# Performance work log

Hardware: AMD Instinct MI355X
Metric: run time of the kernel (lower is better)

The kernel has to match this reference:

```python
import jax, jax.numpy as jnp
import numpy as np

SLOPE = 25.0   # snntorch surrogate.fast_sigmoid default slope
THR = 1.0      # snntorch Leaky default threshold
BETA = 0.95
SPIKE_STEPS = 4
NUM_HEADS = 16

@jax.custom_vjp
def spike(u):
    # Heaviside forward, fast-sigmoid surrogate backward
    return (u > 0).astype(u.dtype)

def _spike_fwd(u):
    return spike(u), u

def _spike_bwd(u, g):
    return (g / (SLOPE * jnp.abs(u) + 1.0) ** 2,)

spike.defvjp(_spike_fwd, _spike_bwd)

def lif_mean(cur):
    """Run SPIKE_STEPS of a snntorch Leaky neuron (subtract reset, detached)
    with constant input current `cur`; return mean spike train over time."""
    def step(mem, _):
        reset = jax.lax.stop_gradient(spike(mem - THR))
        mem = BETA * mem + cur - reset * THR
        return mem, spike(mem - THR)
    _, spk = jax.lax.scan(step, jnp.zeros_like(cur), None, length=SPIKE_STEPS)
    return spk.mean(axis=0)

def setup_inputs() -> dict:
    B, S, D = 2, 2048, 1024
    key = jax.random.key(0)
    ks = jax.random.split(key, 9)
    std = 1.0 / np.sqrt(D)
    mkw = lambda k: jax.random.uniform(k, (D, D), jnp.float32, -std, std)
    mkb = lambda k: jax.random.uniform(k, (D,), jnp.float32, -std, std)
    return {
        "x": jax.random.normal(ks[0], (B, S, D), jnp.float32),
        "q_w": mkw(ks[1]), "q_b": mkb(ks[2]),
        "k_w": mkw(ks[3]), "k_b": mkb(ks[4]),
        "v_w": mkw(ks[5]), "v_b": mkb(ks[6]),
        "o_w": mkw(ks[7]), "o_b": mkb(ks[8]),
    }

def reference(x, q_w, q_b, k_w, k_b, v_w, v_b, o_w, o_b):
    B, S, D = x.shape
    H = NUM_HEADS
    Hd = D // H
    # projections -> [B, H, S, Hd]  (weights stored [in, out])
    proj = lambda w, b: (x @ w + b).reshape(B, S, H, Hd).transpose(0, 2, 1, 3)
    q, k, v = proj(q_w, q_b), proj(k_w, k_b), proj(v_w, v_b)
    # LIF spiking recurrence, aggregated over time
    q_agg, k_agg, v_agg = lif_mean(q), lif_mean(k), lif_mean(v)
    # standard scaled dot-product attention on aggregated spikes
    scores = jnp.einsum('bhqd,bhkd->bhqk', q_agg, k_agg) / jnp.sqrt(jnp.float32(Hd))
    attn = jax.nn.softmax(scores, axis=-1)
    out = jnp.einsum('bhqk,bhkd->bhqd', attn, v_agg)
    out = out.transpose(0, 2, 1, 3).reshape(B, S, D)
    return out @ o_w + o_b
```

## Files before the change

### kernel.cpp

```cpp
#include <hip/hip_runtime.h>
#include <hip/hip_bf16.h>
#include <stdint.h>

typedef unsigned short u16;
typedef unsigned int u32;
typedef __bf16 bf16x8 __attribute__((ext_vector_type(8)));
typedef float f32x4 __attribute__((ext_vector_type(4)));

#define B_   2
#define S_   2048
#define D_   1024
#define H_   16
#define HD_  64

__device__ __forceinline__ u16 f2bf(float f) {
    u32 u = __float_as_uint(f);
    u32 r = (u + 0x7FFFu + ((u >> 16) & 1u)) >> 16;
    return (u16)r;
}
__device__ __forceinline__ float bf2f(u16 s) { return __uint_as_float(((u32)s) << 16); }

__device__ __forceinline__ f32x4 mfma16(bf16x8 a, bf16x8 b, f32x4 c) {
    return __builtin_amdgcn_mfma_f32_16x16x32_bf16(a, b, c, 0, 0, 0);
}

__device__ __forceinline__ void gl16(const u16* g, u16* l) {
    __builtin_amdgcn_global_load_lds(
        (const __attribute__((address_space(1))) void*)g,
        (__attribute__((address_space(3))) void*)l, 16, 0, 0);
}

__global__ void prep_kernel(const float* __restrict__ x,
                            const float* __restrict__ qw, const float* __restrict__ kw,
                            const float* __restrict__ vw, const float* __restrict__ ow,
                            u16* __restrict__ xbf, u16* __restrict__ wt_all) {
    __shared__ float tile[32][33];
    const int bid = blockIdx.x;
    const int t = threadIdx.x;
    if (bid < 4096) {
        int i = bid * 256 + t;
        float4 v = reinterpret_cast<const float4*>(x)[i];
        uint2 hp;
        hp.x = (u32)f2bf(v.x) | ((u32)f2bf(v.y) << 16);
        hp.y = (u32)f2bf(v.z) | ((u32)f2bf(v.w) << 16);
        reinterpret_cast<uint2*>(xbf)[i] = hp;
        return;
    }
    const int f = bid - 4096;
    const int z = f >> 10;
    const int bi = (f & 1023) >> 5;
    const int bj = f & 31;
    const float* w = (z == 0) ? qw : (z == 1) ? kw : (z == 2) ? vw : ow;
    u16* thi = wt_all + (size_t)z * 1048576;
    const int tx = t & 31, ty = t >> 5;
#pragma unroll
    for (int k = 0; k < 4; k++) {
        int r = ty + k * 8;
        tile[r][tx] = w[(size_t)(bi * 32 + r) * D_ + bj * 32 + tx];
    }
    __syncthreads();
#pragma unroll
    for (int k = 0; k < 4; k++) {
        int r = ty + k * 8;
        thi[(size_t)(bj * 32 + r) * D_ + bi * 32 + tx] = f2bf(tile[tx][r]);
    }
}

__global__ __launch_bounds__(256, 3)
void qkv_gemm(const u16* __restrict__ Ag, const u16* __restrict__ Bg,
              const float* __restrict__ qb, const float* __restrict__ kb,
              const float* __restrict__ vb,
              u16* __restrict__ o0, u16* __restrict__ o1, u16* __restrict__ o2) {
    __shared__ __align__(16) u16 lA[2][128 * 32];
    __shared__ __align__(16) u16 lB[2][128 * 32];

    const int t = threadIdx.x;
    const int flat = blockIdx.y * 24 + blockIdx.x;
    const int swz = (flat & 7) * 96 + (flat >> 3);
    const int m0 = (swz / 24) * 128;
    const int n0 = (swz % 24) * 128;
    const int wid = t >> 6, lane = t & 63;
    const int wm = wid >> 1, wn = wid & 1;
    const int lr = lane & 15, lg = lane >> 4;

    f32x4 acc[4][4] = {};

    auto STAGE = [&](int buf, int kk) {
        const int k0 = kk * 32;
#pragma unroll
        for (int p = 0; p < 2; p++) {
            int idx = p * 256 + wid * 64 + lane;
            int row = idx >> 2, sl = idx & 3;
            int slx = sl ^ ((row >> 1) & 3);
            gl16(Ag + (size_t)(m0 + row) * D_ + k0 + slx * 8,
                 &lA[buf][(p * 256 + wid * 64) * 8]);
            gl16(Bg + (size_t)(n0 + row) * D_ + k0 + slx * 8,
                 &lB[buf][(p * 256 + wid * 64) * 8]);
        }
    };

    STAGE(0, 0);
    __syncthreads();
    int cur = 0;

    for (int kk = 0; kk < 32; ++kk) {
        if (kk < 31) STAGE(cur ^ 1, kk + 1);

        bf16x8 af[4], bf[4];
#pragma unroll
        for (int m = 0; m < 4; m++) {
            int row = wm * 64 + m * 16 + lr;
            af[m] = *reinterpret_cast<const bf16x8*>(
                &lA[cur][row * 32 + (lg ^ ((row >> 1) & 3)) * 8]);
        }
#pragma unroll
        for (int n = 0; n < 4; n++) {
            int row = wn * 64 + n * 16 + lr;
            bf[n] = *reinterpret_cast<const bf16x8*>(
                &lB[cur][row * 32 + (lg ^ ((row >> 1) & 3)) * 8]);
        }
#pragma unroll
        for (int m = 0; m < 4; m++)
#pragma unroll
            for (int n = 0; n < 4; n++)
                acc[m][n] = mfma16(af[m], bf[n], acc[m][n]);

        __syncthreads();
        cur ^= 1;
    }

    const int col0f = n0 + wn * 64;
    const int proj = col0f >> 10;
    const float* bp = (proj == 0) ? qb : (proj == 1) ? kb : vb;
    u16* dst = (proj == 0) ? o0 : (proj == 1) ? o1 : o2;
#pragma unroll
    for (int m = 0; m < 4; m++) {
#pragma unroll
        for (int n = 0; n < 4; n++) {
            u16 agg4[4];
#pragma unroll
            for (int r = 0; r < 4; r++) {
                int row = m0 + wm * 64 + m * 16 + lg * 4 + r;
                int colp = (col0f + n * 16 + lr) & 1023;
                float cur_i = acc[m][n][r] + bp[colp];
                float mem = 0.f;
                int cnt = 0;
#pragma unroll
                for (int tt = 0; tt < 4; tt++) {
                    float reset = (mem > 1.f) ? 1.f : 0.f;
                    mem = 0.95f * mem;
                    mem = mem + cur_i;
                    mem = mem - reset;
                    cnt += (mem > 1.f) ? 1 : 0;
                }
                u16 agg = (u16)(__float_as_uint((float)cnt * 0.25f) >> 16);
                if (proj != 2) {
                    int b = row >> 11, s = row & 2047;
                    int h = colp >> 6, d = colp & 63;
                    dst[((size_t)(b * H_ + h) * S_ + s) * HD_ + d] = agg;
                } else {
                    agg4[r] = agg;
                }
            }
            if (proj == 2) {
                int row0 = m0 + wm * 64 + m * 16 + lg * 4;
                int colp = (col0f + n * 16 + lr) & 1023;
                int b = row0 >> 11, s = row0 & 2047;
                int h = colp >> 6, d = colp & 63;
                uint2 pk;
                pk.x = (u32)agg4[0] | ((u32)agg4[1] << 16);
                pk.y = (u32)agg4[2] | ((u32)agg4[3] << 16);
                *reinterpret_cast<uint2*>(
                    &dst[((size_t)(b * H_ + h) * HD_ + d) * S_ + s]) = pk;
            }
        }
    }
}

__global__ __launch_bounds__(256, 4)
void o_gemm(const u16* __restrict__ Ag, const u16* __restrict__ Bhg,
            const float* __restrict__ bias, float* __restrict__ out) {
    __shared__ __align__(16) u16 lA[2][64 * 32];
    __shared__ __align__(16) u16 lB[2][64 * 32];

    const int t = threadIdx.x;
    const int flat = blockIdx.y * 16 + blockIdx.x;
    const int swz = (flat & 7) * 128 + (flat >> 3);
    const int m0 = (swz >> 4) * 64;
    const int n0 = (swz & 15) * 64;
    const int wid = t >> 6, lane = t & 63;
    const int wm = wid >> 1, wn = wid & 1;
    const int lr = lane & 15, lg = lane >> 4;

    f32x4 acc[2][2] = {};

    auto STAGE = [&](int buf, int kk) {
        const int k0 = kk * 32;
        int idx = wid * 64 + lane;
        int row = idx >> 2, sl = idx & 3;
        int slx = sl ^ ((row >> 1) & 3);
        gl16(Ag + (size_t)(m0 + row) * D_ + k0 + slx * 8,
             &lA[buf][(wid * 64) * 8]);
        gl16(Bhg + (size_t)(n0 + row) * D_ + k0 + slx * 8,
             &lB[buf][(wid * 64) * 8]);
    };

    STAGE(0, 0);
    __syncthreads();
    int cur = 0;

    for (int kk = 0; kk < 32; ++kk) {
        if (kk < 31) STAGE(cur ^ 1, kk + 1);

        bf16x8 af[2], bf[2];
#pragma unroll
        for (int m = 0; m < 2; m++) {
            int row = wm * 32 + m * 16 + lr;
            af[m] = *reinterpret_cast<const bf16x8*>(
                &lA[cur][row * 32 + (lg ^ ((row >> 1) & 3)) * 8]);
        }
#pragma unroll
        for (int n = 0; n < 2; n++) {
            int row = wn * 32 + n * 16 + lr;
            bf[n] = *reinterpret_cast<const bf16x8*>(
                &lB[cur][row * 32 + (lg ^ ((row >> 1) & 3)) * 8]);
        }
#pragma unroll
        for (int m = 0; m < 2; m++)
#pragma unroll
            for (int n = 0; n < 2; n++)
                acc[m][n] = mfma16(af[m], bf[n], acc[m][n]);

        __syncthreads();
        cur ^= 1;
    }

#pragma unroll
    for (int m = 0; m < 2; m++)
#pragma unroll
        for (int n = 0; n < 2; n++)
#pragma unroll
            for (int r = 0; r < 4; r++) {
                int row = m0 + wm * 32 + m * 16 + lg * 4 + r;
                int col = n0 + wn * 32 + n * 16 + lr;
                out[(size_t)row * D_ + col] = acc[m][n][r] + bias[col];
            }
}

__global__ __launch_bounds__(256, 3)
void attn_kernel(const u16* __restrict__ qa, const u16* __restrict__ ka,
                 const u16* __restrict__ vt, u16* __restrict__ oag) {
    __shared__ __align__(16) u16 Kb[2][64 * 64];
    __shared__ __align__(16) u16 Vb[2][64 * 64];
    __shared__ __align__(16) u16 Pt[4][32 * 64];

    const int t = threadIdx.x;
    const int wid = t >> 6, lane = t & 63;
    const int lr = lane & 15, lg = lane >> 4;

    const int flat = blockIdx.y * 16 + blockIdx.x;
    const int swz = (flat & 7) * 64 + (flat >> 3);
    const int bh = swz >> 4;
    const int q0 = (swz & 15) * 128;

    const u16* qbase = qa + (size_t)bh * S_ * HD_;
    const u16* kbase = ka + (size_t)bh * S_ * HD_;
    const u16* vbase = vt + (size_t)bh * HD_ * S_;

    bf16x8 qf[2][2];
#pragma unroll
    for (int m = 0; m < 2; m++)
#pragma unroll
        for (int kc = 0; kc < 2; kc++) {
            int row = q0 + wid * 32 + m * 16 + lr;
            qf[m][kc] = *reinterpret_cast<const bf16x8*>(
                qbase + (size_t)row * HD_ + kc * 32 + lg * 8);
        }

    bf16x8 ones;
#pragma unroll
    for (int j = 0; j < 8; j++) ones[j] = (__bf16)1.0f;

    f32x4 oacc[2][4] = {};
    f32x4 ssum[2] = {};
    u16* myP = &Pt[wid][0];

    auto STAGE = [&](int buf, int kt) {
#pragma unroll
        for (int p = 0; p < 2; p++) {
            int slot = p * 256 + wid * 64 + lane;
            int row = slot >> 3, sl = slot & 7;
            int slx = sl ^ (row & 7);
            gl16(kbase + (size_t)(kt * 64 + row) * HD_ + slx * 8,
                 &Kb[buf][(p * 256 + wid * 64) * 8]);
            gl16(vbase + (size_t)row * S_ + kt * 64 + slx * 8,
                 &Vb[buf][(p * 256 + wid * 64) * 8]);
        }
    };

    STAGE(0, 0);
    __syncthreads();
    int cur = 0;

    for (int kt = 0; kt < 32; ++kt) {
        if (kt < 31) STAGE(cur ^ 1, kt + 1);

        f32x4 sacc[2][4] = {};
        __builtin_amdgcn_s_setprio(1);
#pragma unroll
        for (int n = 0; n < 4; n++) {
            int row = n * 16 + lr;
#pragma unroll
            for (int kc = 0; kc < 2; kc++) {
                int sl = kc * 4 + lg;
                bf16x8 kb = *reinterpret_cast<const bf16x8*>(
                    &Kb[cur][row * 64 + ((sl ^ (row & 7)) * 8)]);
                sacc[0][n] = mfma16(qf[0][kc], kb, sacc[0][n]);
                sacc[1][n] = mfma16(qf[1][kc], kb, sacc[1][n]);
            }
        }
        __builtin_amdgcn_s_setprio(0);
        char* pbase = reinterpret_cast<char*>(myP);
#pragma unroll
        for (int m = 0; m < 2; m++)
#pragma unroll
            for (int n = 0; n < 4; n++) {
                float pv[4];
#pragma unroll
                for (int r = 0; r < 4; r++) {
                    float tt = __builtin_fmaf(sacc[m][n][r], 0.18033688f,
                                              -5.7707802f);
                    asm("v_exp_f32 %0, %1" : "=v"(pv[r]) : "v"(tt));
                }
                u32 d01, d23;
                asm("v_cvt_pk_bf16_f32 %0, %1, %2"
                    : "=v"(d01) : "v"(pv[0]), "v"(pv[1]));
                asm("v_cvt_pk_bf16_f32 %0, %1, %2"
                    : "=v"(d23) : "v"(pv[2]), "v"(pv[3]));
                const int pr = m * 16 + lg * 4;
                const int cb = (n * 16 + lr) * 2;
                *reinterpret_cast<u16*>(pbase + (pr + 0) * 128 +
                                        (cb ^ (((pr + 0) & 7) << 4))) = (u16)d01;
                *reinterpret_cast<u16*>(pbase + (pr + 1) * 128 +
                                        (cb ^ (((pr + 1) & 7) << 4))) = (u16)(d01 >> 16);
                *reinterpret_cast<u16*>(pbase + (pr + 2) * 128 +
                                        (cb ^ (((pr + 2) & 7) << 4))) = (u16)d23;
                *reinterpret_cast<u16*>(pbase + (pr + 3) * 128 +
                                        (cb ^ (((pr + 3) & 7) << 4))) = (u16)(d23 >> 16);
            }
        bf16x8 pa[2][2];
#pragma unroll
        for (int m = 0; m < 2; m++)
#pragma unroll
            for (int kc = 0; kc < 2; kc++) {
                int row = m * 16 + lr;
                int sl = kc * 4 + lg;
                pa[m][kc] = *reinterpret_cast<const bf16x8*>(
                    &myP[row * 64 + ((sl ^ (row & 7)) * 8)]);
            }
        __builtin_amdgcn_s_setprio(1);
#pragma unroll
        for (int n = 0; n < 4; n++) {
            int row = n * 16 + lr;
#pragma unroll
            for (int kc = 0; kc < 2; kc++) {
                int sl = kc * 4 + lg;
                bf16x8 vb = *reinterpret_cast<const bf16x8*>(
                    &Vb[cur][row * 64 + ((sl ^ (row & 7)) * 8)]);
                oacc[0][n] = mfma16(pa[0][kc], vb, oacc[0][n]);
                oacc[1][n] = mfma16(pa[1][kc], vb, oacc[1][n]);
            }
        }
        ssum[0] = mfma16(pa[0][0], ones, ssum[0]);
        ssum[0] = mfma16(pa[0][1], ones, ssum[0]);
        ssum[1] = mfma16(pa[1][0], ones, ssum[1]);
        ssum[1] = mfma16(pa[1][1], ones, ssum[1]);
        __builtin_amdgcn_s_setprio(0);

        __syncthreads();
        cur ^= 1;
    }

    const int b = bh >> 4, h = bh & 15;
#pragma unroll
    for (int m = 0; m < 2; m++)
#pragma unroll
        for (int n = 0; n < 4; n++)
#pragma unroll
            for (int r = 0; r < 4; r++) {
                int q = q0 + wid * 32 + m * 16 + lg * 4 + r;
                int d = n * 16 + lr;
                float v = oacc[m][n][r] / ssum[m][r];
                oag[(size_t)(b * S_ + q) * D_ + h * 64 + d] = f2bf(v);
            }
}

extern "C" void kernel_launch(void* const* d_in, const int* in_sizes, int n_in,
                              void* d_out, int out_size, void* d_ws, size_t ws_size,
                              hipStream_t stream) {
    (void)in_sizes; (void)n_in; (void)out_size; (void)ws_size;
    const float* x  = (const float*)d_in[0];
    const float* qw = (const float*)d_in[1];
    const float* qb = (const float*)d_in[2];
    const float* kw = (const float*)d_in[3];
    const float* kb = (const float*)d_in[4];
    const float* vw = (const float*)d_in[5];
    const float* vb = (const float*)d_in[6];
    const float* ow = (const float*)d_in[7];
    const float* ob = (const float*)d_in[8];

    u16* ws = (u16*)d_ws;
    const size_t C = 4194304;
    u16* xbf = ws + 0 * C;
    u16* wt  = ws + 1 * C;
    u16* qag = ws + 2 * C;
    u16* kag = ws + 3 * C;
    u16* vtg = ws + 4 * C;
    u16* oag = ws + 5 * C;

    prep_kernel<<<8192, 256, 0, stream>>>(x, qw, kw, vw, ow, xbf, wt);

    qkv_gemm<<<dim3(24, 32), 256, 0, stream>>>(
        xbf, wt, qb, kb, vb, qag, kag, vtg);
    attn_kernel<<<dim3(16, 32), 256, 0, stream>>>(qag, kag, vtg, oag);
    o_gemm<<<dim3(16, 64), 256, 0, stream>>>(
        oag, wt + 3 * 1048576, ob, (float*)d_out);
}
```

Measured before the change: 121.4 us.

## Triple-buffer LDS staging with vmcnt waits in GEMM and attention kernels

Moves the QKV GEMM, output GEMM and attention kernels from double-buffered to triple-buffered LDS tiles. Each kernel now prefetches two stages ahead, waits with explicit s_waitcnt vmcnt counts and uses one barrier per iteration instead of two syncthreads. The aim is to hide global-load latency behind more MFMA work. It costs more LDS per block, and the attention kernel's launch bounds drop from 3 to 2 blocks per SM, so occupancy may fall. The wait_vm helper is added but never called.

```diff
diff --git a/kernel.cpp b/kernel.cpp
--- a/kernel.cpp
+++ b/kernel.cpp
@@ -28,6 +28,18 @@
     __builtin_amdgcn_global_load_lds(
         (const __attribute__((address_space(1))) void*)g,
         (__attribute__((address_space(3))) void*)l, 16, 0, 0);
+}
+
+__device__ __forceinline__ void wait_vm(int t, int last, int midN) {
+    if (t < last - 1) {
+        if (midN == 4) asm volatile("s_waitcnt vmcnt(4)" ::: "memory");
+        else           asm volatile("s_waitcnt vmcnt(2)" ::: "memory");
+    } else if (t == last - 1) {
+        if (midN == 4) asm volatile("s_waitcnt vmcnt(4)" ::: "memory");
+        else           asm volatile("s_waitcnt vmcnt(2)" ::: "memory");
+    } else {
+        asm volatile("s_waitcnt vmcnt(0)" ::: "memory");
+    }
 }
 
 __global__ void prep_kernel(const float* __restrict__ x,
@@ -71,8 +83,8 @@
               const float* __restrict__ qb, const float* __restrict__ kb,
               const float* __restrict__ vb,
               u16* __restrict__ o0, u16* __restrict__ o1, u16* __restrict__ o2) {
-    __shared__ __align__(16) u16 lA[2][128 * 32];
-    __shared__ __align__(16) u16 lB[2][128 * 32];
+    __shared__ __align__(16) u16 lA[3][128 * 32];
+    __shared__ __align__(16) u16 lB[3][128 * 32];
 
     const int t = threadIdx.x;
     const int flat = blockIdx.y * 24 + blockIdx.x;
@@ -100,12 +112,15 @@
     };
 
     STAGE(0, 0);
-    __syncthreads();
-    int cur = 0;
+    STAGE(1, 1);
 
     for (int kk = 0; kk < 32; ++kk) {
-        if (kk < 31) STAGE(cur ^ 1, kk + 1);
-
+        if (kk < 31) asm volatile("s_waitcnt vmcnt(4)" ::: "memory");
+        else         asm volatile("s_waitcnt vmcnt(0)" ::: "memory");
+        __builtin_amdgcn_s_barrier();
+        if (kk < 30) STAGE((kk + 2) % 3, kk + 2);
+
+        const int cur = kk % 3;
         bf16x8 af[4], bf[4];
 #pragma unroll
         for (int m = 0; m < 4; m++) {
@@ -124,9 +139,6 @@
 #pragma unroll
             for (int n = 0; n < 4; n++)
                 acc[m][n] = mfma16(af[m], bf[n], acc[m][n]);
-
-        __syncthreads();
-        cur ^= 1;
     }
 
     const int col0f = n0 + wn * 64;
@@ -180,8 +192,8 @@
 __global__ __launch_bounds__(256, 4)
 void o_gemm(const u16* __restrict__ Ag, const u16* __restrict__ Bhg,
             const float* __restrict__ bias, float* __restrict__ out) {
-    __shared__ __align__(16) u16 lA[2][64 * 32];
-    __shared__ __align__(16) u16 lB[2][64 * 32];
+    __shared__ __align__(16) u16 lA[3][64 * 32];
+    __shared__ __align__(16) u16 lB[3][64 * 32];
 
     const int t = threadIdx.x;
     const int flat = blockIdx.y * 16 + blockIdx.x;
@@ -206,12 +218,15 @@
     };
 
     STAGE(0, 0);
-    __syncthreads();
-    int cur = 0;
+    STAGE(1, 1);
 
     for (int kk = 0; kk < 32; ++kk) {
-        if (kk < 31) STAGE(cur ^ 1, kk + 1);
-
+        if (kk < 31) asm volatile("s_waitcnt vmcnt(2)" ::: "memory");
+        else         asm volatile("s_waitcnt vmcnt(0)" ::: "memory");
+        __builtin_amdgcn_s_barrier();
+        if (kk < 30) STAGE((kk + 2) % 3, kk + 2);
+
+        const int cur = kk % 3;
         bf16x8 af[2], bf[2];
 #pragma unroll
         for (int m = 0; m < 2; m++) {
@@ -230,9 +245,6 @@
 #pragma unroll
             for (int n = 0; n < 2; n++)
                 acc[m][n] = mfma16(af[m], bf[n], acc[m][n]);
-
-        __syncthreads();
-        cur ^= 1;
     }
 
 #pragma unroll
@@ -247,11 +259,11 @@
             }
 }
 
-__global__ __launch_bounds__(256, 3)
+__global__ __launch_bounds__(256, 2)
 void attn_kernel(const u16* __restrict__ qa, const u16* __restrict__ ka,
                  const u16* __restrict__ vt, u16* __restrict__ oag) {
-    __shared__ __align__(16) u16 Kb[2][64 * 64];
-    __shared__ __align__(16) u16 Vb[2][64 * 64];
+    __shared__ __align__(16) u16 Kb[3][64 * 64];
+    __shared__ __align__(16) u16 Vb[3][64 * 64];
     __shared__ __align__(16) u16 Pt[4][32 * 64];
 
     const int t = threadIdx.x;
@@ -299,12 +311,15 @@
     };
 
     STAGE(0, 0);
-    __syncthreads();
-    int cur = 0;
+    STAGE(1, 1);
 
     for (int kt = 0; kt < 32; ++kt) {
-        if (kt < 31) STAGE(cur ^ 1, kt + 1);
-
+        if (kt < 31) asm volatile("s_waitcnt vmcnt(4)" ::: "memory");
+        else         asm volatile("s_waitcnt vmcnt(0)" ::: "memory");
+        __builtin_amdgcn_s_barrier();
+        if (kt < 30) STAGE((kt + 2) % 3, kt + 2);
+
+        const int cur = kt % 3;
         f32x4 sacc[2][4] = {};
         __builtin_amdgcn_s_setprio(1);
 #pragma unroll
@@ -376,9 +391,6 @@
         ssum[1] = mfma16(pa[1][0], ones, ssum[1]);
         ssum[1] = mfma16(pa[1][1], ones, ssum[1]);
         __builtin_amdgcn_s_setprio(0);
-
-        __syncthreads();
-        cur ^= 1;
     }
 
     const int b = bh >> 4, h = bh & 15;
```

Measured after the change: 117.4 us. -3.3%, faster.
